# Optimization experiments

Measured on AMD Instinct MI355X. Metric: run time of the kernel, lower is better.

Reference implementation:

```python
import jax, jax.numpy as jnp
import numpy as np

N_NODES = 100000
N_EDGES = 1600000
N_GRAPHS = 2048
EPS = 1e-5


def gcn_conv(x, src, dst, W, b):
    # PyG GCNConv: add self-loops, symmetric normalization D^-1/2 (A+I) D^-1/2, then linear.
    xw = x @ W  # [N, F]
    deg = jax.ops.segment_sum(jnp.ones((src.shape[0],), xw.dtype), dst, num_segments=N_NODES) + 1.0
    dinv = jax.lax.rsqrt(deg)  # deg >= 1 due to self loops
    norm = dinv[src] * dinv[dst]  # [E]
    msg = xw[src] * norm[:, None]  # gather + scale
    agg = jax.ops.segment_sum(msg, dst, num_segments=N_NODES)
    agg = agg + xw * (dinv * dinv)[:, None]  # self-loop term
    return agg + b


def bn_eval(h, gamma, beta, rm, rv):
    return (h - rm) * jax.lax.rsqrt(rv + EPS) * gamma + beta


def setup_inputs() -> dict:
    key = jax.random.key(0)
    ks = jax.random.split(key, 12)
    x = jax.random.normal(ks[0], (N_NODES, 74), jnp.float32)
    edge_index = jax.random.randint(ks[1], (2, N_EDGES), 0, N_NODES, dtype=jnp.int64)
    batch = jnp.sort(jax.random.randint(ks[2], (N_NODES,), 0, N_GRAPHS, dtype=jnp.int64))
    def lin(k, fi, fo):
        return jax.random.normal(k, (fi, fo), jnp.float32) / np.sqrt(fi)
    return {
        "x": x, "edge_index": edge_index, "batch": batch,
        "W1": lin(ks[3], 74, 256), "b1": jnp.zeros((256,), jnp.float32),
        "g1": jnp.ones((256,), jnp.float32), "beta1": jnp.zeros((256,), jnp.float32),
        "rm1": jax.random.normal(ks[4], (256,), jnp.float32) * 0.1,
        "rv1": jax.random.uniform(ks[5], (256,), jnp.float32, 0.5, 1.5),
        "W2": lin(ks[6], 256, 256), "b2": jnp.zeros((256,), jnp.float32),
        "g2": jnp.ones((256,), jnp.float32), "beta2": jnp.zeros((256,), jnp.float32),
        "rm2": jax.random.normal(ks[7], (256,), jnp.float32) * 0.1,
        "rv2": jax.random.uniform(ks[8], (256,), jnp.float32, 0.5, 1.5),
        "W3": lin(ks[9], 256, 384), "b3": jnp.zeros((384,), jnp.float32),
    }


def reference(x, edge_index, batch, W1, b1, g1, beta1, rm1, rv1,
              W2, b2, g2, beta2, rm2, rv2, W3, b3):
    src, dst = edge_index[0], edge_index[1]
    h1 = jax.nn.relu(bn_eval(gcn_conv(x, src, dst, W1, b1), g1, beta1, rm1, rv1))
    h2 = jax.nn.relu(bn_eval(gcn_conv(h1, src, dst, W2, b2), g2, beta2, rm2, rv2))
    h3 = gcn_conv(h2, src, dst, W3, b3)
    # global_mean_pool + global_max_pool over batch segments
    cnt = jax.ops.segment_sum(jnp.ones((N_NODES,), h3.dtype), batch, num_segments=N_GRAPHS)
    mean_pool = jax.ops.segment_sum(h3, batch, num_segments=N_GRAPHS) / jnp.maximum(cnt, 1.0)[:, None]
    max_pool = jax.ops.segment_max(h3, batch, num_segments=N_GRAPHS)
    return mean_pool + max_pool
```

## Files before the change

kernel.cpp:

```cpp
#include <hip/hip_runtime.h>

typedef __bf16 bf16x8 __attribute__((ext_vector_type(8)));
typedef float f32x4 __attribute__((ext_vector_type(4)));
typedef unsigned short ushort4v __attribute__((ext_vector_type(4)));
typedef unsigned short ushort8v __attribute__((ext_vector_type(8)));

__device__ __forceinline__ unsigned short f2b(float f) {
  unsigned u = __float_as_uint(f);
  unsigned r = u + 0x7FFFu + ((u >> 16) & 1u);
  return (unsigned short)(r >> 16);
}
__device__ __forceinline__ float b2f(unsigned short v) {
  return __uint_as_float(((unsigned)v) << 16);
}

static constexpr int SCAN_CHUNK = 1024;

__global__ void k_bnprep(const float* __restrict__ g, const float* __restrict__ beta,
                         const float* __restrict__ rm, const float* __restrict__ rv,
                         const float* __restrict__ b, int n,
                         float* __restrict__ scale, float* __restrict__ shift) {
  int i = blockIdx.x * blockDim.x + threadIdx.x;
  if (i < n) {
    float s = g[i] * rsqrtf(rv[i] + 1e-5f);
    scale[i] = s;
    shift[i] = (b[i] - rm[i]) * s + beta[i];
  }
}

__global__ void k_edge_count(const int* __restrict__ dst, int E, int* __restrict__ cnt) {
  int i = blockIdx.x * blockDim.x + threadIdx.x;
  if (i < E) atomicAdd(&cnt[dst[i]], 1);
}

__global__ void k_dinv(const int* __restrict__ cnt, int n, float* __restrict__ dinv) {
  int i = blockIdx.x * blockDim.x + threadIdx.x;
  if (i < n) dinv[i] = rsqrtf(1.0f + (float)cnt[i]);
}

__global__ void k_wt(const float* __restrict__ W, int K, int N, int Kp,
                     unsigned short* __restrict__ Wt) {
  int idx = blockIdx.x * blockDim.x + threadIdx.x;
  if (idx >= N * Kp) return;
  int n = idx / Kp, k = idx - n * Kp;
  Wt[idx] = f2b(k < K ? W[(size_t)k * N + n] : 0.0f);
}

__global__ void k_x2b(const float* __restrict__ x, int n, unsigned short* __restrict__ xb) {
  int idx = blockIdx.x * blockDim.x + threadIdx.x;
  if (idx >= n * 20) return;
  int row = idx / 20, j = idx - row * 20;
  int f0 = j * 4;
  ushort4v o;
#pragma unroll
  for (int j2 = 0; j2 < 4; ++j2) {
    int f = f0 + j2;
    o[j2] = (f < 74) ? f2b(x[(size_t)row * 74 + f]) : (unsigned short)0;
  }
  *(ushort4v*)(xb + (size_t)row * 80 + f0) = o;
}

__global__ void k_gbounds(const int* __restrict__ batch, int n, int* __restrict__ gstart,
                          int* __restrict__ gend) {
  int i = blockIdx.x * blockDim.x + threadIdx.x;
  if (i >= n) return;
  int g = batch[i];
  if (i == 0 || batch[i - 1] != g) gstart[g] = i;
  if (i == n - 1 || batch[i + 1] != g) gend[g] = i + 1;
}

__global__ void k_chunk_sum(const int* __restrict__ cnt, int n, int* __restrict__ bsum) {
  __shared__ int s[256];
  int base = blockIdx.x * SCAN_CHUNK;
  int t = threadIdx.x;
  int v = 0;
  for (int i = t; i < SCAN_CHUNK; i += 256) {
    int idx = base + i;
    v += (idx < n) ? cnt[idx] : 0;
  }
  s[t] = v;
  __syncthreads();
  for (int o = 128; o > 0; o >>= 1) {
    if (t < o) s[t] += s[t + o];
    __syncthreads();
  }
  if (t == 0) bsum[blockIdx.x] = s[0];
}

__global__ void k_scan_bsum(int* __restrict__ bsum, int nb) {
  if (threadIdx.x == 0 && blockIdx.x == 0) {
    int acc = 0;
    for (int i = 0; i < nb; ++i) { int v = bsum[i]; bsum[i] = acc; acc += v; }
  }
}

__global__ void k_write_rowptr(const int* __restrict__ cnt, int n, const int* __restrict__ bsum,
                               int* __restrict__ rowptr, int E) {
  __shared__ int s[256];
  __shared__ int sx[257];
  int base = blockIdx.x * SCAN_CHUNK;
  int t = threadIdx.x;
  int loc[4];
  int sum = 0;
#pragma unroll
  for (int j = 0; j < 4; ++j) {
    int idx = base + t * 4 + j;
    int c = (idx < n) ? cnt[idx] : 0;
    loc[j] = sum;
    sum += c;
  }
  s[t] = sum;
  __syncthreads();
  if (t == 0) {
    int acc = 0;
    for (int i = 0; i < 256; ++i) { sx[i] = acc; acc += s[i]; }
  }
  __syncthreads();
  int off = bsum[blockIdx.x] + sx[t];
#pragma unroll
  for (int j = 0; j < 4; ++j) {
    int idx = base + t * 4 + j;
    if (idx < n) rowptr[idx] = off + loc[j];
  }
  if (blockIdx.x == 0 && t == 0) rowptr[n] = E;
}

__global__ void k_fill(const int* __restrict__ src, const int* __restrict__ dst, int E,
                       const int* __restrict__ rowptr, int* __restrict__ cursor,
                       const float* __restrict__ dinv, int* __restrict__ col,
                       float* __restrict__ wt) {
  int e = blockIdx.x * blockDim.x + threadIdx.x;
  if (e < E) {
    int d = dst[e], s = src[e];
    int p = atomicAdd(&cursor[d], 1);
    int idx = rowptr[d] + p;
    col[idx] = s;
    wt[idx] = dinv[s] * dinv[d];
  }
}

__global__ __launch_bounds__(256) void k_aggregate74b(const unsigned short* __restrict__ xb,
                                                      const int* __restrict__ rowptr,
                                                      const int* __restrict__ col,
                                                      const float* __restrict__ wt,
                                                      const float* __restrict__ dinv, int n,
                                                      unsigned short* __restrict__ out) {
  int wid = (int)((blockIdx.x * (size_t)blockDim.x + threadIdx.x) >> 6);
  int lane = threadIdx.x & 63;
  if (wid >= n) return;
  int half = lane >> 5, hl = lane & 31;
  bool act = hl < 20;
  float acc[4] = {0.0f, 0.0f, 0.0f, 0.0f};
  int e0 = rowptr[wid], e1 = rowptr[wid + 1];
  int e = e0;
  for (; e + 3 < e1; e += 4) {
    int me0 = e + half * 2, me1 = me0 + 1;
    int s0 = col[me0], s1 = col[me1];
    float w0 = wt[me0], w1 = wt[me1];
    ushort4v v0 = {}, v1 = {};
    if (act) {
      v0 = *(const ushort4v*)(xb + (size_t)s0 * 80 + hl * 4);
      v1 = *(const ushort4v*)(xb + (size_t)s1 * 80 + hl * 4);
    }
#pragma unroll
    for (int j = 0; j < 4; ++j)
      acc[j] += w0 * b2f(v0[j]) + w1 * b2f(v1[j]);
  }
  for (int t = e + half; t < e1; t += 2) {
    int s = col[t];
    float w = wt[t];
    ushort4v v = {};
    if (act) v = *(const ushort4v*)(xb + (size_t)s * 80 + hl * 4);
#pragma unroll
    for (int j = 0; j < 4; ++j) acc[j] += w * b2f(v[j]);
  }
#pragma unroll
  for (int j = 0; j < 4; ++j) acc[j] += __shfl_xor(acc[j], 32);
  if (half == 0) {
    float di = dinv[wid];
    float sw = di * di;
    if (act) {
      ushort4v sv = *(const ushort4v*)(xb + (size_t)wid * 80 + hl * 4);
      ushort4v o;
#pragma unroll
      for (int j = 0; j < 4; ++j) o[j] = f2b(acc[j] + sw * b2f(sv[j]));
      *(ushort4v*)(out + (size_t)wid * 128 + hl * 4) = o;
    } else {
      ushort4v z = {};
      *(ushort4v*)(out + (size_t)wid * 128 + 80 + (hl - 20) * 4) = z;
    }
  }
}

__global__ __launch_bounds__(256) void k_aggregate256(const unsigned short* __restrict__ in,
                                                      const int* __restrict__ rowptr,
                                                      const int* __restrict__ col,
                                                      const float* __restrict__ wt,
                                                      const float* __restrict__ dinv, int n,
                                                      unsigned short* __restrict__ out) {
  int wid = (int)((blockIdx.x * (size_t)blockDim.x + threadIdx.x) >> 6);
  int lane = threadIdx.x & 63;
  if (wid >= n) return;
  float di = dinv[wid];
  float sw = di * di;
  ushort4v sv = *(const ushort4v*)(in + (size_t)wid * 256 + lane * 4);
  float acc[4];
#pragma unroll
  for (int j = 0; j < 4; ++j) acc[j] = sw * b2f(sv[j]);
  int e0 = rowptr[wid], e1 = rowptr[wid + 1];
  int e = e0;
  for (; e + 3 < e1; e += 4) {
    int s0 = col[e], s1 = col[e + 1], s2 = col[e + 2], s3 = col[e + 3];
    float w0 = wt[e], w1 = wt[e + 1], w2 = wt[e + 2], w3 = wt[e + 3];
    ushort4v v0 = *(const ushort4v*)(in + (size_t)s0 * 256 + lane * 4);
    ushort4v v1 = *(const ushort4v*)(in + (size_t)s1 * 256 + lane * 4);
    ushort4v v2 = *(const ushort4v*)(in + (size_t)s2 * 256 + lane * 4);
    ushort4v v3 = *(const ushort4v*)(in + (size_t)s3 * 256 + lane * 4);
#pragma unroll
    for (int j = 0; j < 4; ++j)
      acc[j] += w0 * b2f(v0[j]) + w1 * b2f(v1[j]) + w2 * b2f(v2[j]) + w3 * b2f(v3[j]);
  }
  for (; e < e1; ++e) {
    int s = col[e];
    float w = wt[e];
    ushort4v v = *(const ushort4v*)(in + (size_t)s * 256 + lane * 4);
#pragma unroll
    for (int j = 0; j < 4; ++j) acc[j] += w * b2f(v[j]);
  }
  ushort4v o;
#pragma unroll
  for (int j = 0; j < 4; ++j) o[j] = f2b(acc[j]);
  *(ushort4v*)(out + (size_t)wid * 256 + lane * 4) = o;
}

template <int EPI>
__global__ __launch_bounds__(256) void k_gemm_mfma(const unsigned short* __restrict__ A,
                                                   const unsigned short* __restrict__ Bt,
                                                   int M, int N, int K,
                                                   const float* __restrict__ scale,
                                                   const float* __restrict__ shift,
                                                   unsigned short* __restrict__ C) {
  __shared__ __align__(16) unsigned short Ast[128 * 64];
  __shared__ __align__(16) unsigned short Bst[64 * 64];
  const int t = threadIdx.x;
  const int lane = t & 63;
  const int wid = t >> 6;
  const int wm = wid >> 1, wn = wid & 1;
  const int lr = lane >> 4, lc = lane & 15;
  const int m0 = blockIdx.y * 128;
  const int n0 = blockIdx.x * 64;
  f32x4 acc[4][2] = {};
  char* astB = (char*)Ast;
  char* bstB = (char*)Bst;

  for (int kb = 0; kb < K; kb += 64) {
#pragma unroll
    for (int i = 0; i < 4; ++i) {
      int c = t + 256 * i;
      int row = c >> 3, slot = c & 7;
      int gm = m0 + row;
      ushort8v v = {};
      if (gm < M) v = *(const ushort8v*)(A + (size_t)gm * K + kb + slot * 8);
      int byte = row * 128 + slot * 16;
      *(ushort8v*)(astB + (byte ^ ((row & 7) << 4))) = v;
    }
#pragma unroll
    for (int i = 0; i < 2; ++i) {
      int c = t + 256 * i;
      int row = c >> 3, slot = c & 7;
      ushort8v v = *(const ushort8v*)(Bt + (size_t)(n0 + row) * K + kb + slot * 8);
      int byte = row * 128 + slot * 16;
      *(ushort8v*)(bstB + (byte ^ ((row & 7) << 4))) = v;
    }
    __syncthreads();
#pragma unroll
    for (int kk = 0; kk < 2; ++kk) {
      bf16x8 a[4], b[2];
      int kbyte = lr * 16 + kk * 64;
#pragma unroll
      for (int mi = 0; mi < 4; ++mi) {
        int row = wm * 64 + mi * 16 + lc;
        int byte = row * 128 + kbyte;
        a[mi] = *(const bf16x8*)(astB + (byte ^ ((row & 7) << 4)));
      }
#pragma unroll
      for (int ni = 0; ni < 2; ++ni) {
        int row = wn * 32 + ni * 16 + lc;
        int byte = row * 128 + kbyte;
        b[ni] = *(const bf16x8*)(bstB + (byte ^ ((row & 7) << 4)));
      }
#pragma unroll
      for (int mi = 0; mi < 4; ++mi)
#pragma unroll
        for (int ni = 0; ni < 2; ++ni)
          acc[mi][ni] =
              __builtin_amdgcn_mfma_f32_16x16x32_bf16(a[mi], b[ni], acc[mi][ni], 0, 0, 0);
    }
    __syncthreads();
  }

#pragma unroll
  for (int ni = 0; ni < 2; ++ni) {
    int colx = n0 + wn * 32 + ni * 16 + lc;
    float sc = (EPI == 0) ? scale[colx] : 0.0f;
    float sh = shift[colx];
#pragma unroll
    for (int mi = 0; mi < 4; ++mi) {
      int rbase = m0 + wm * 64 + mi * 16 + lr * 4;
#pragma unroll
      for (int r = 0; r < 4; ++r) {
        int row = rbase + r;
        if (row < M) {
          float v = acc[mi][ni][r];
          if (EPI == 0) v = fmaxf(fmaf(v, sc, sh), 0.0f);
          else v += sh;
          C[(size_t)row * N + colx] = f2b(v);
        }
      }
    }
  }
}

__global__ __launch_bounds__(384) void k_pool(const unsigned short* __restrict__ h3,
                                              const int* __restrict__ gstart,
                                              const int* __restrict__ gend, int NF,
                                              float* __restrict__ out) {
  int g = blockIdx.x;
  int t = threadIdx.x;
  int s = gstart[g], e = gend[g];
  if (s >= 0 && e > s) {
    float sum = 0.0f, mx = -3.4e38f;
    for (int r = s; r < e; ++r) {
      float v = b2f(h3[(size_t)r * NF + t]);
      sum += v;
      mx = fmaxf(mx, v);
    }
    out[(size_t)g * NF + t] = sum / (float)(e - s) + mx;
  } else {
    out[(size_t)g * NF + t] = -INFINITY;
  }
}

extern "C" void kernel_launch(void* const* d_in, const int* in_sizes, int n_in, void* d_out,
                              int out_size, void* d_ws, size_t ws_size, hipStream_t stream) {
  const float* x    = (const float*)d_in[0];
  const int* edge   = (const int*)d_in[1];
  const int* batch  = (const int*)d_in[2];
  const float* W1   = (const float*)d_in[3];
  const float* b1   = (const float*)d_in[4];
  const float* g1   = (const float*)d_in[5];
  const float* be1  = (const float*)d_in[6];
  const float* rm1  = (const float*)d_in[7];
  const float* rv1  = (const float*)d_in[8];
  const float* W2   = (const float*)d_in[9];
  const float* b2   = (const float*)d_in[10];
  const float* g2   = (const float*)d_in[11];
  const float* be2  = (const float*)d_in[12];
  const float* rm2  = (const float*)d_in[13];
  const float* rv2  = (const float*)d_in[14];
  const float* W3   = (const float*)d_in[15];
  const float* b3   = (const float*)d_in[16];

  const int NN = in_sizes[2];
  const int E  = in_sizes[1] / 2;
  const int F1 = in_sizes[4];
  const int F3 = in_sizes[16];
  const int NG = out_size / F3;
  const int K1p = 128;
  const int* srcv = edge;
  const int* dstv = edge + E;

  char* p = (char*)d_ws;
  auto carve = [&](size_t bytes) -> char* {
    char* r = p;
    p += (bytes + 255) & ~(size_t)255;
    return r;
  };
  float* dinv           = (float*)carve((size_t)NN * 4);
  int* cnt              = (int*)carve((size_t)NN * 4);
  int* rowptr           = (int*)carve((size_t)(NN + 1) * 4);
  int* cursor           = (int*)carve((size_t)NN * 4);
  int* bsum             = (int*)carve(4096);
  int* col              = (int*)carve((size_t)E * 4);
  float* wt             = (float*)carve((size_t)E * 4);
  float* scale1         = (float*)carve((size_t)F1 * 4);
  float* shift1         = (float*)carve((size_t)F1 * 4);
  float* scale2         = (float*)carve((size_t)F1 * 4);
  float* shift2         = (float*)carve((size_t)F1 * 4);
  unsigned short* W1t   = (unsigned short*)carve((size_t)F1 * K1p * 2);
  unsigned short* W2t   = (unsigned short*)carve((size_t)F1 * F1 * 2);
  unsigned short* W3t   = (unsigned short*)carve((size_t)F3 * F1 * 2);
  int* gstart           = (int*)carve((size_t)NG * 4);
  int* gend             = (int*)carve((size_t)NG * 4);
  unsigned short* xb    = (unsigned short*)carve((size_t)NN * 80 * 2);
  unsigned short* agg   = (unsigned short*)carve((size_t)NN * F1 * 2);
  unsigned short* h     = (unsigned short*)carve((size_t)NN * F1 * 2);
  unsigned short* h3    = (unsigned short*)carve((size_t)NN * F3 * 2);
  (void)ws_size; (void)n_in;

  hipMemsetAsync(cnt, 0, (size_t)NN * 4, stream);
  hipMemsetAsync(cursor, 0, (size_t)NN * 4, stream);
  hipMemsetAsync(gstart, 0xFF, (size_t)NG * 4, stream);
  hipMemsetAsync(gend, 0, (size_t)NG * 4, stream);
  k_bnprep<<<1, 256, 0, stream>>>(g1, be1, rm1, rv1, b1, F1, scale1, shift1);
  k_bnprep<<<1, 256, 0, stream>>>(g2, be2, rm2, rv2, b2, F1, scale2, shift2);
  k_wt<<<(F1 * K1p + 255) / 256, 256, 0, stream>>>(W1, 74, F1, K1p, W1t);
  k_wt<<<(F1 * F1 + 255) / 256, 256, 0, stream>>>(W2, F1, F1, F1, W2t);
  k_wt<<<(F3 * F1 + 255) / 256, 256, 0, stream>>>(W3, F1, F3, F1, W3t);
  k_x2b<<<(NN * 20 + 255) / 256, 256, 0, stream>>>(x, NN, xb);
  k_gbounds<<<(NN + 255) / 256, 256, 0, stream>>>(batch, NN, gstart, gend);

  k_edge_count<<<(E + 255) / 256, 256, 0, stream>>>(dstv, E, cnt);
  k_dinv<<<(NN + 255) / 256, 256, 0, stream>>>(cnt, NN, dinv);
  int nchunks = (NN + SCAN_CHUNK - 1) / SCAN_CHUNK;
  k_chunk_sum<<<nchunks, 256, 0, stream>>>(cnt, NN, bsum);
  k_scan_bsum<<<1, 64, 0, stream>>>(bsum, nchunks);
  k_write_rowptr<<<nchunks, 256, 0, stream>>>(cnt, NN, bsum, rowptr, E);
  k_fill<<<(E + 255) / 256, 256, 0, stream>>>(srcv, dstv, E, rowptr, cursor, dinv, col, wt);

  dim3 blk(256);
  int aggBlocks = (NN + 3) / 4;
  int gy = (NN + 127) / 128;

  k_aggregate74b<<<aggBlocks, blk, 0, stream>>>(xb, rowptr, col, wt, dinv, NN, agg);
  {
    dim3 grid(F1 / 64, gy);
    k_gemm_mfma<0><<<grid, blk, 0, stream>>>(agg, W1t, NN, F1, K1p, scale1, shift1, h);
  }
  k_aggregate256<<<aggBlocks, blk, 0, stream>>>(h, rowptr, col, wt, dinv, NN, agg);
  {
    dim3 grid(F1 / 64, gy);
    k_gemm_mfma<0><<<grid, blk, 0, stream>>>(agg, W2t, NN, F1, F1, scale2, shift2, h);
  }
  k_aggregate256<<<aggBlocks, blk, 0, stream>>>(h, rowptr, col, wt, dinv, NN, agg);
  {
    dim3 grid(F3 / 64, gy);
    k_gemm_mfma<1><<<grid, blk, 0, stream>>>(agg, W3t, NN, F3, F1, nullptr, b3, h3);
  }
  k_pool<<<NG, 384, 0, stream>>>(h3, gstart, gend, F3, (float*)d_out);
}
```

Baseline: 842.8 us.

## Fold GCN normalization into node features and store hidden activations as FP8

Splits the symmetric normalization D^-1/2 A D^-1/2 so the source-side dinv is applied once per node: in the input conversion for layer 1 and in the GEMM epilogue for later layers. The destination-side dinv is applied once at the end of aggregation. This drops the per-edge weight array and its loads. The hidden activations fed to the 256-wide aggregations are stored as FP8 E4M3 instead of bf16, halving the gather bytes per edge, and the aggregation loops are unrolled to 8 edges. The trade is much lower precision in the intermediate features, which risks accuracy tolerance.

```diff
diff --git a/kernel.cpp b/kernel.cpp
--- a/kernel.cpp
+++ b/kernel.cpp
@@ -2,6 +2,7 @@
 
 typedef __bf16 bf16x8 __attribute__((ext_vector_type(8)));
 typedef float f32x4 __attribute__((ext_vector_type(4)));
+typedef float f32x2 __attribute__((ext_vector_type(2)));
 typedef unsigned short ushort4v __attribute__((ext_vector_type(4)));
 typedef unsigned short ushort8v __attribute__((ext_vector_type(8)));
 
@@ -12,6 +13,45 @@
 }
 __device__ __forceinline__ float b2f(unsigned short v) {
   return __uint_as_float(((unsigned)v) << 16);
+}
+
+__device__ __forceinline__ void fp8x4_to_f32(unsigned w, float out[4]) {
+#if __has_builtin(__builtin_amdgcn_cvt_pk_f32_fp8)
+  f32x2 lo = __builtin_amdgcn_cvt_pk_f32_fp8(w, false);
+  f32x2 hi = __builtin_amdgcn_cvt_pk_f32_fp8(w, true);
+  out[0] = lo[0]; out[1] = lo[1]; out[2] = hi[0]; out[3] = hi[1];
+#else
+#pragma unroll
+  for (int i = 0; i < 4; ++i) {
+    unsigned u = (w >> (8 * i)) & 0xffu;
+    unsigned em = u & 0x7fu;
+    float nrm = __uint_as_float((em + 960u) << 20);
+    float sub = (float)em * 0x1p-9f;
+    float mag = (em >= 8u) ? nrm : sub;
+    out[i] = (u & 0x80u) ? -mag : mag;
+  }
+#endif
+}
+
+__device__ __forceinline__ unsigned char f32_to_fp8(float f) {
+  float a = fabsf(f);
+  unsigned s = (__float_as_uint(f) >> 31) << 7;
+  a = fminf(a, 448.0f);
+  unsigned r;
+  if (a >= 0x1p-6f) {
+    unsigned b = __float_as_uint(a);
+    unsigned m = b & 0x7fffffu;
+    int ei = (int)(b >> 23) - 127;
+    unsigned mr = (m + 0x80000u) >> 20;
+    unsigned ee = (unsigned)(ei + 7) + (mr >> 3);
+    mr &= 7u;
+    if (ee >= 16u) { ee = 15u; mr = 6u; }
+    r = (ee << 3) | mr;
+  } else {
+    unsigned m = (unsigned)(a * 512.0f + 0.5f);
+    r = m;
+  }
+  return (unsigned char)(s | r);
 }
 
 static constexpr int SCAN_CHUNK = 1024;
@@ -46,16 +86,18 @@
   Wt[idx] = f2b(k < K ? W[(size_t)k * N + n] : 0.0f);
 }
 
-__global__ void k_x2b(const float* __restrict__ x, int n, unsigned short* __restrict__ xb) {
+__global__ void k_x2b(const float* __restrict__ x, const float* __restrict__ dinv, int n,
+                      unsigned short* __restrict__ xb) {
   int idx = blockIdx.x * blockDim.x + threadIdx.x;
   if (idx >= n * 20) return;
   int row = idx / 20, j = idx - row * 20;
   int f0 = j * 4;
+  float dv = dinv[row];
   ushort4v o;
 #pragma unroll
   for (int j2 = 0; j2 < 4; ++j2) {
     int f = f0 + j2;
-    o[j2] = (f < 74) ? f2b(x[(size_t)row * 74 + f]) : (unsigned short)0;
+    o[j2] = (f < 74) ? f2b(dv * x[(size_t)row * 74 + f]) : (unsigned short)0;
   }
   *(ushort4v*)(xb + (size_t)row * 80 + f0) = o;
 }
@@ -127,22 +169,18 @@
 
 __global__ void k_fill(const int* __restrict__ src, const int* __restrict__ dst, int E,
                        const int* __restrict__ rowptr, int* __restrict__ cursor,
-                       const float* __restrict__ dinv, int* __restrict__ col,
-                       float* __restrict__ wt) {
+                       int* __restrict__ colA) {
   int e = blockIdx.x * blockDim.x + threadIdx.x;
   if (e < E) {
-    int d = dst[e], s = src[e];
+    int d = dst[e];
     int p = atomicAdd(&cursor[d], 1);
-    int idx = rowptr[d] + p;
-    col[idx] = s;
-    wt[idx] = dinv[s] * dinv[d];
+    colA[rowptr[d] + p] = src[e];
   }
 }
 
 __global__ __launch_bounds__(256) void k_aggregate74b(const unsigned short* __restrict__ xb,
                                                       const int* __restrict__ rowptr,
-                                                      const int* __restrict__ col,
-                                                      const float* __restrict__ wt,
+                                                      const int* __restrict__ colA,
                                                       const float* __restrict__ dinv, int n,
                                                       unsigned short* __restrict__ out) {
   int wid = (int)((blockIdx.x * (size_t)blockDim.x + threadIdx.x) >> 6);
@@ -153,37 +191,36 @@
   float acc[4] = {0.0f, 0.0f, 0.0f, 0.0f};
   int e0 = rowptr[wid], e1 = rowptr[wid + 1];
   int e = e0;
-  for (; e + 3 < e1; e += 4) {
-    int me0 = e + half * 2, me1 = me0 + 1;
-    int s0 = col[me0], s1 = col[me1];
-    float w0 = wt[me0], w1 = wt[me1];
-    ushort4v v0 = {}, v1 = {};
+  for (; e + 7 < e1; e += 8) {
+    int b = e + half * 4;
+    int s0 = colA[b], s1 = colA[b + 1], s2 = colA[b + 2], s3 = colA[b + 3];
+    ushort4v v0 = {}, v1 = {}, v2 = {}, v3 = {};
     if (act) {
       v0 = *(const ushort4v*)(xb + (size_t)s0 * 80 + hl * 4);
       v1 = *(const ushort4v*)(xb + (size_t)s1 * 80 + hl * 4);
+      v2 = *(const ushort4v*)(xb + (size_t)s2 * 80 + hl * 4);
+      v3 = *(const ushort4v*)(xb + (size_t)s3 * 80 + hl * 4);
     }
 #pragma unroll
     for (int j = 0; j < 4; ++j)
-      acc[j] += w0 * b2f(v0[j]) + w1 * b2f(v1[j]);
+      acc[j] += (b2f(v0[j]) + b2f(v1[j])) + (b2f(v2[j]) + b2f(v3[j]));
   }
   for (int t = e + half; t < e1; t += 2) {
-    int s = col[t];
-    float w = wt[t];
+    int s = colA[t];
     ushort4v v = {};
     if (act) v = *(const ushort4v*)(xb + (size_t)s * 80 + hl * 4);
 #pragma unroll
-    for (int j = 0; j < 4; ++j) acc[j] += w * b2f(v[j]);
+    for (int j = 0; j < 4; ++j) acc[j] += b2f(v[j]);
   }
 #pragma unroll
   for (int j = 0; j < 4; ++j) acc[j] += __shfl_xor(acc[j], 32);
   if (half == 0) {
     float di = dinv[wid];
-    float sw = di * di;
     if (act) {
       ushort4v sv = *(const ushort4v*)(xb + (size_t)wid * 80 + hl * 4);
       ushort4v o;
 #pragma unroll
-      for (int j = 0; j < 4; ++j) o[j] = f2b(acc[j] + sw * b2f(sv[j]));
+      for (int j = 0; j < 4; ++j) o[j] = f2b(di * (acc[j] + b2f(sv[j])));
       *(ushort4v*)(out + (size_t)wid * 128 + hl * 4) = o;
     } else {
       ushort4v z = {};
@@ -192,44 +229,48 @@
   }
 }
 
-__global__ __launch_bounds__(256) void k_aggregate256(const unsigned short* __restrict__ in,
+__global__ __launch_bounds__(256) void k_aggregate256(const unsigned char* __restrict__ h8,
                                                       const int* __restrict__ rowptr,
-                                                      const int* __restrict__ col,
-                                                      const float* __restrict__ wt,
+                                                      const int* __restrict__ colA,
                                                       const float* __restrict__ dinv, int n,
                                                       unsigned short* __restrict__ out) {
   int wid = (int)((blockIdx.x * (size_t)blockDim.x + threadIdx.x) >> 6);
   int lane = threadIdx.x & 63;
   if (wid >= n) return;
-  float di = dinv[wid];
-  float sw = di * di;
-  ushort4v sv = *(const ushort4v*)(in + (size_t)wid * 256 + lane * 4);
   float acc[4];
-#pragma unroll
-  for (int j = 0; j < 4; ++j) acc[j] = sw * b2f(sv[j]);
+  {
+    unsigned w = *(const unsigned*)(h8 + (size_t)wid * 256 + lane * 4);
+    fp8x4_to_f32(w, acc);
+  }
   int e0 = rowptr[wid], e1 = rowptr[wid + 1];
   int e = e0;
-  for (; e + 3 < e1; e += 4) {
-    int s0 = col[e], s1 = col[e + 1], s2 = col[e + 2], s3 = col[e + 3];
-    float w0 = wt[e], w1 = wt[e + 1], w2 = wt[e + 2], w3 = wt[e + 3];
-    ushort4v v0 = *(const ushort4v*)(in + (size_t)s0 * 256 + lane * 4);
-    ushort4v v1 = *(const ushort4v*)(in + (size_t)s1 * 256 + lane * 4);
-    ushort4v v2 = *(const ushort4v*)(in + (size_t)s2 * 256 + lane * 4);
-    ushort4v v3 = *(const ushort4v*)(in + (size_t)s3 * 256 + lane * 4);
-#pragma unroll
-    for (int j = 0; j < 4; ++j)
-      acc[j] += w0 * b2f(v0[j]) + w1 * b2f(v1[j]) + w2 * b2f(v2[j]) + w3 * b2f(v3[j]);
+  for (; e + 7 < e1; e += 8) {
+    int c[8];
+    unsigned w[8];
+#pragma unroll
+    for (int q = 0; q < 8; ++q) c[q] = colA[e + q];
+#pragma unroll
+    for (int q = 0; q < 8; ++q)
+      w[q] = *(const unsigned*)(h8 + (size_t)c[q] * 256 + lane * 4);
+#pragma unroll
+    for (int q = 0; q < 8; ++q) {
+      float v[4];
+      fp8x4_to_f32(w[q], v);
+#pragma unroll
+      for (int j = 0; j < 4; ++j) acc[j] += v[j];
+    }
   }
   for (; e < e1; ++e) {
-    int s = col[e];
-    float w = wt[e];
-    ushort4v v = *(const ushort4v*)(in + (size_t)s * 256 + lane * 4);
-#pragma unroll
-    for (int j = 0; j < 4; ++j) acc[j] += w * b2f(v[j]);
-  }
+    unsigned w = *(const unsigned*)(h8 + (size_t)colA[e] * 256 + lane * 4);
+    float v[4];
+    fp8x4_to_f32(w, v);
+#pragma unroll
+    for (int j = 0; j < 4; ++j) acc[j] += v[j];
+  }
+  float di = dinv[wid];
   ushort4v o;
 #pragma unroll
-  for (int j = 0; j < 4; ++j) o[j] = f2b(acc[j]);
+  for (int j = 0; j < 4; ++j) o[j] = f2b(di * acc[j]);
   *(ushort4v*)(out + (size_t)wid * 256 + lane * 4) = o;
 }
 
@@ -239,7 +280,9 @@
                                                    int M, int N, int K,
                                                    const float* __restrict__ scale,
                                                    const float* __restrict__ shift,
-                                                   unsigned short* __restrict__ C) {
+                                                   const float* __restrict__ dinv,
+                                                   unsigned char* __restrict__ C8,
+                                                   unsigned short* __restrict__ C16) {
   __shared__ __align__(16) unsigned short Ast[128 * 64];
   __shared__ __align__(16) unsigned short Bst[64 * 64];
   const int t = threadIdx.x;
@@ -312,9 +355,13 @@
         int row = rbase + r;
         if (row < M) {
           float v = acc[mi][ni][r];
-          if (EPI == 0) v = fmaxf(fmaf(v, sc, sh), 0.0f);
-          else v += sh;
-          C[(size_t)row * N + colx] = f2b(v);
+          if (EPI == 0) {
+            v = fmaxf(fmaf(v, sc, sh), 0.0f) * dinv[row];
+            C8[(size_t)row * N + colx] = f32_to_fp8(v);
+          } else {
+            v += sh;
+            C16[(size_t)row * N + colx] = f2b(v);
+          }
         }
       }
     }
@@ -381,8 +428,7 @@
   int* rowptr           = (int*)carve((size_t)(NN + 1) * 4);
   int* cursor           = (int*)carve((size_t)NN * 4);
   int* bsum             = (int*)carve(4096);
-  int* col              = (int*)carve((size_t)E * 4);
-  float* wt             = (float*)carve((size_t)E * 4);
+  int* colA             = (int*)carve((size_t)E * 4);
   float* scale1         = (float*)carve((size_t)F1 * 4);
   float* shift1         = (float*)carve((size_t)F1 * 4);
   float* scale2         = (float*)carve((size_t)F1 * 4);
@@ -393,8 +439,8 @@
   int* gstart           = (int*)carve((size_t)NG * 4);
   int* gend             = (int*)carve((size_t)NG * 4);
   unsigned short* xb    = (unsigned short*)carve((size_t)NN * 80 * 2);
+  unsigned char* h8     = (unsigned char*)carve((size_t)NN * F1);
   unsigned short* agg   = (unsigned short*)carve((size_t)NN * F1 * 2);
-  unsigned short* h     = (unsigned short*)carve((size_t)NN * F1 * 2);
   unsigned short* h3    = (unsigned short*)carve((size_t)NN * F3 * 2);
   (void)ws_size; (void)n_in;
 
@@ -407,35 +453,39 @@
   k_wt<<<(F1 * K1p + 255) / 256, 256, 0, stream>>>(W1, 74, F1, K1p, W1t);
   k_wt<<<(F1 * F1 + 255) / 256, 256, 0, stream>>>(W2, F1, F1, F1, W2t);
   k_wt<<<(F3 * F1 + 255) / 256, 256, 0, stream>>>(W3, F1, F3, F1, W3t);
-  k_x2b<<<(NN * 20 + 255) / 256, 256, 0, stream>>>(x, NN, xb);
   k_gbounds<<<(NN + 255) / 256, 256, 0, stream>>>(batch, NN, gstart, gend);
 
   k_edge_count<<<(E + 255) / 256, 256, 0, stream>>>(dstv, E, cnt);
   k_dinv<<<(NN + 255) / 256, 256, 0, stream>>>(cnt, NN, dinv);
+  k_x2b<<<(NN * 20 + 255) / 256, 256, 0, stream>>>(x, dinv, NN, xb);
+
   int nchunks = (NN + SCAN_CHUNK - 1) / SCAN_CHUNK;
   k_chunk_sum<<<nchunks, 256, 0, stream>>>(cnt, NN, bsum);
   k_scan_bsum<<<1, 64, 0, stream>>>(bsum, nchunks);
   k_write_rowptr<<<nchunks, 256, 0, stream>>>(cnt, NN, bsum, rowptr, E);
-  k_fill<<<(E + 255) / 256, 256, 0, stream>>>(srcv, dstv, E, rowptr, cursor, dinv, col, wt);
+  k_fill<<<(E + 255) / 256, 256, 0, stream>>>(srcv, dstv, E, rowptr, cursor, colA);
 
   dim3 blk(256);
   int aggBlocks = (NN + 3) / 4;
   int gy = (NN + 127) / 128;
 
-  k_aggregate74b<<<aggBlocks, blk, 0, stream>>>(xb, rowptr, col, wt, dinv, NN, agg);
+  k_aggregate74b<<<aggBlocks, blk, 0, stream>>>(xb, rowptr, colA, dinv, NN, agg);
   {
     dim3 grid(F1 / 64, gy);
-    k_gemm_mfma<0><<<grid, blk, 0, stream>>>(agg, W1t, NN, F1, K1p, scale1, shift1, h);
-  }
-  k_aggregate256<<<aggBlocks, blk, 0, stream>>>(h, rowptr, col, wt, dinv, NN, agg);
+    k_gemm_mfma<0><<<grid, blk, 0, stream>>>(agg, W1t, NN, F1, K1p, scale1, shift1, dinv,
+                                             h8, nullptr);
+  }
+  k_aggregate256<<<aggBlocks, blk, 0, stream>>>(h8, rowptr, colA, dinv, NN, agg);
   {
     dim3 grid(F1 / 64, gy);
-    k_gemm_mfma<0><<<grid, blk, 0, stream>>>(agg, W2t, NN, F1, F1, scale2, shift2, h);
-  }
-  k_aggregate256<<<aggBlocks, blk, 0, stream>>>(h, rowptr, col, wt, dinv, NN, agg);
+    k_gemm_mfma<0><<<grid, blk, 0, stream>>>(agg, W2t, NN, F1, F1, scale2, shift2, dinv,
+                                             h8, nullptr);
+  }
+  k_aggregate256<<<aggBlocks, blk, 0, stream>>>(h8, rowptr, colA, dinv, NN, agg);
   {
     dim3 grid(F3 / 64, gy);
-    k_gemm_mfma<1><<<grid, blk, 0, stream>>>(agg, W3t, NN, F3, F1, nullptr, b3, h3);
+    k_gemm_mfma<1><<<grid, blk, 0, stream>>>(agg, W3t, NN, F3, F1, nullptr, b3, dinv,
+                                             nullptr, h3);
   }
   k_pool<<<NG, 384, 0, stream>>>(h3, gstart, gend, F3, (float*)d_out);
 }
```

Measured after the change: 744.5 us. 11.7% less time.
